# Kernel tuning notes

Measured on AMD Instinct MI355X. Metric: run time of the kernel, lower is better.

The kernel has to match this reference:

```python
import jax, jax.numpy as jnp
import numpy as np

N_AGENTS = 8
OBS = 64          # num_inputs // n_agents
HIDDEN = 128
NUM_OUT = 16
BATCH = 16384     # per-agent batch -> rows = BATCH * N_AGENTS = 131072


def setup_inputs() -> dict:
    key = jax.random.key(0)
    ks = jax.random.split(key, 9)
    s = lambda fan_in: 1.0 / np.sqrt(fan_in)
    inputs = jax.random.normal(ks[0], (BATCH * N_AGENTS, OBS), dtype=jnp.float32)
    w1  = jax.random.uniform(ks[1], (HIDDEN, OBS), jnp.float32, -s(OBS), s(OBS))
    b1  = jax.random.uniform(ks[2], (HIDDEN,), jnp.float32, -s(OBS), s(OBS))
    w1o = jax.random.uniform(ks[3], (HIDDEN, OBS), jnp.float32, -s(OBS), s(OBS))
    b1o = jax.random.uniform(ks[4], (HIDDEN,), jnp.float32, -s(OBS), s(OBS))
    w2  = jax.random.uniform(ks[5], (HIDDEN, 2 * HIDDEN), jnp.float32, -s(2 * HIDDEN), s(2 * HIDDEN))
    b2  = jax.random.uniform(ks[6], (HIDDEN,), jnp.float32, -s(2 * HIDDEN), s(2 * HIDDEN))
    wv  = jax.random.uniform(ks[7], (NUM_OUT, HIDDEN), jnp.float32, -s(HIDDEN), s(HIDDEN)) * 0.1
    bv  = jax.random.uniform(ks[8], (NUM_OUT,), jnp.float32, -s(HIDDEN), s(HIDDEN)) * 0.1
    return {"inputs": inputs, "w1": w1, "b1": b1, "w1o": w1o, "b1o": b1o,
            "w2": w2, "b2": b2, "wv": wv, "bv": bv}


def reference(inputs, w1, b1, w1o, b1o, w2, b2, wv, bv):
    n = N_AGENTS
    B = inputs.shape[0] // n
    obs = inputs.shape[1]
    # state_other: roll features by -1, then for each of n iterations take
    # [B, n, obs][:, 1:] and roll again (faithful to torch.roll/cat loop).
    rolled = jnp.roll(inputs, -1, axis=1)
    parts = []
    for _ in range(n):  # fixed small structural loop
        parts.append(rolled.reshape(B, n, obs)[:, 1:])
        rolled = jnp.roll(rolled, -1, axis=1)
    state_other = jnp.concatenate(parts, axis=1).reshape(B * n, n - 1, obs)

    h1 = jax.nn.relu(inputs @ w1.T + b1)                                   # [B*n, H]
    h1_other = jax.nn.relu(jnp.einsum('bno,ho->bnh', state_other, w1o) + b1o)  # [B*n, n-1, H]
    h1_summed = jnp.sum(h1_other, axis=1) / n                              # [B*n, H]
    h = jnp.concatenate([h1, h1_summed], axis=1)                           # [B*n, 2H]
    h2 = jax.nn.relu(h @ w2.T + b2)                                        # [B*n, H]
    return h2 @ wv.T + bv                                                  # [B*n, num_out]
```

## Files before the change

### kernel.cpp

```cpp
#include <hip/hip_runtime.h>
#include <stdint.h>
#include <stddef.h>


typedef __attribute__((ext_vector_type(8))) short short8;
typedef __attribute__((ext_vector_type(4))) float floatx4;
typedef __attribute__((ext_vector_type(4))) unsigned int uintx4;
typedef __attribute__((ext_vector_type(4))) float float4v;

static __device__ __forceinline__ unsigned int cvtpk(float lo, float hi) {
    unsigned int r;
    asm("v_cvt_pk_bf16_f32 %0, %1, %2" : "=v"(r) : "v"(lo), "v"(hi));
    return r;
}
static __device__ __forceinline__ unsigned short f2bf(float f) {
    return (unsigned short)cvtpk(f, f);
}

static __device__ __forceinline__ floatx4 mfma16(short8 a, short8 b, floatx4 c) {
    return __builtin_amdgcn_mfma_f32_16x16x32_bf16(a, b, c, 0, 0, 0);
}

__global__ void cvt_weights(const float* __restrict__ w1, const float* __restrict__ w1o,
                            const float* __restrict__ w2, const float* __restrict__ wv,
                            unsigned short* __restrict__ ws) {
    int i = blockIdx.x * 256 + threadIdx.x;
    float v;
    if (i < 8192)       v = w1[i];
    else if (i < 16384) v = w1o[i - 8192];
    else if (i < 49152) v = w2[i - 16384];
    else                v = wv[i - 49152];
    ws[i] = f2bf(v);
}

__launch_bounds__(256, 3)
__global__ void actor_fused(const float* __restrict__ X,
                            const unsigned short* __restrict__ ws,
                            const float* __restrict__ b1p,
                            const float* __restrict__ b1op,
                            const float* __restrict__ b2p,
                            const float* __restrict__ bvp,
                            float* __restrict__ out) {
    __shared__ __align__(16) unsigned char smem[51200];
    unsigned short (*Hc)[264] = (unsigned short (*)[264])(smem);
    unsigned short (*Xs)[72]  = (unsigned short (*)[72]) (smem + 33792);
    unsigned short (*H2)[136] = (unsigned short (*)[136])(smem + 33792);

    const int tid  = threadIdx.x;
    const int wid  = tid >> 6;
    const int lane = tid & 63;
    const int l15  = lane & 15;
    const int l16  = lane >> 4;
    const long R0  = (long)blockIdx.x * 64;

    const unsigned short* w1b  = ws;
    const unsigned short* w1ob = ws + 8192;
    const unsigned short* w2b  = ws + 16384;
    const unsigned short* wvb  = ws + 49152;

    short8 bo[8][2];
    float b1o_r[8];
    #pragma unroll
    for (int n = 0; n < 8; ++n) {
        const int h = n * 16 + l15;
        bo[n][0] = *(const short8*)(w1ob + h * 64 + l16 * 8);
        bo[n][1] = *(const short8*)(w1ob + h * 64 + 32 + l16 * 8);
        b1o_r[n] = b1op[h];
    }

    {
        const int r = tid >> 2, q = tid & 3;
        const float4v* src = (const float4v*)(X + (R0 + r) * 64 + q * 16);
        const float4v f0 = src[0], f1 = src[1], f2 = src[2], f3 = src[3];
        uintx4 lo, hi;
        lo.x = cvtpk(f0.x, f0.y); lo.y = cvtpk(f0.z, f0.w);
        lo.z = cvtpk(f1.x, f1.y); lo.w = cvtpk(f1.z, f1.w);
        hi.x = cvtpk(f2.x, f2.y); hi.y = cvtpk(f2.z, f2.w);
        hi.z = cvtpk(f3.x, f3.y); hi.w = cvtpk(f3.z, f3.w);
        *(uintx4*)(&Xs[r][q * 16])     = lo;
        *(uintx4*)(&Xs[r][q * 16 + 8]) = hi;
        if (q == 0) *(uintx4*)(&Xs[r][64]) = lo;
    }
    __syncthreads();

    const int xrow = 16 * wid + l15;
    uintx4 v0lo = *(const uintx4*)(&Xs[xrow][l16 * 8]);
    uintx4 v0hi = *(const uintx4*)(&Xs[xrow][l16 * 8 + 8]);
    uintx4 v1lo = *(const uintx4*)(&Xs[xrow][32 + l16 * 8]);
    uintx4 v1hi = *(const uintx4*)(&Xs[xrow][40 + l16 * 8]);
    unsigned int u0[8] = {v0lo.x, v0lo.y, v0lo.z, v0lo.w, v0hi.x, v0hi.y, v0hi.z, v0hi.w};
    unsigned int u1[8] = {v1lo.x, v1lo.y, v1lo.z, v1lo.w, v1hi.x, v1hi.y, v1hi.z, v1hi.w};

    const floatx4 zf = {0.f, 0.f, 0.f, 0.f};

    #pragma unroll
    for (int kx = 0; kx < 8; ++kx) {
        const int kk = kx + 1;
        const int c  = kk >> 1;
        union { unsigned int u[4]; short8 v; } A0, A1;
        #pragma unroll
        for (int d = 0; d < 4; ++d) {
            if (kk & 1) {
                A0.u[d] = (u0[d + c] >> 16) | (u0[d + c + 1] << 16);
                A1.u[d] = (u1[d + c] >> 16) | (u1[d + c + 1] << 16);
            } else {
                A0.u[d] = u0[d + c];
                A1.u[d] = u1[d + c];
            }
        }
        floatx4 acc[8];
        #pragma unroll
        for (int n = 0; n < 8; ++n) acc[n] = zf;
        #pragma unroll
        for (int n = 0; n < 8; ++n) {
            acc[n] = mfma16(A0.v, bo[n][0], acc[n]);
            acc[n] = mfma16(A1.v, bo[n][1], acc[n]);
        }
        #pragma unroll
        for (int n = 0; n < 8; ++n) {
            float r0 = fmaxf(acc[n].x + b1o_r[n], 0.f);
            float r1 = fmaxf(acc[n].y + b1o_r[n], 0.f);
            float r2 = fmaxf(acc[n].z + b1o_r[n], 0.f);
            float r3 = fmaxf(acc[n].w + b1o_r[n], 0.f);
            float t = r1 + r2 + r3 + (((l16 & 1) != 0) ? r0 : 0.f);
            float s = t + __shfl_xor(t, 16, 64);
            if ((lane & 16) == 0) {
                int row = 16 * wid + ((lane >> 5) << 3) + kx;
                Hc[row][128 + n * 16 + l15] = f2bf(s * 0.125f);
            }
        }
    }

    {
        short8 b1fr[8][2];
        float b1_r[8];
        #pragma unroll
        for (int n = 0; n < 8; ++n) {
            const int h = n * 16 + l15;
            b1fr[n][0] = *(const short8*)(w1b + h * 64 + l16 * 8);
            b1fr[n][1] = *(const short8*)(w1b + h * 64 + 32 + l16 * 8);
            b1_r[n]    = b1p[h];
        }
        union { unsigned int u[4]; short8 v; } A0, A1;
        #pragma unroll
        for (int d = 0; d < 4; ++d) { A0.u[d] = u0[d]; A1.u[d] = u1[d]; }
        floatx4 acc[8];
        #pragma unroll
        for (int n = 0; n < 8; ++n) acc[n] = zf;
        #pragma unroll
        for (int n = 0; n < 8; ++n) {
            acc[n] = mfma16(A0.v, b1fr[n][0], acc[n]);
            acc[n] = mfma16(A1.v, b1fr[n][1], acc[n]);
        }
        #pragma unroll
        for (int n = 0; n < 8; ++n) {
            #pragma unroll
            for (int r = 0; r < 4; ++r) {
                int row = 16 * wid + l16 * 4 + r;
                Hc[row][n * 16 + l15] = f2bf(fmaxf(acc[n][r] + b1_r[n], 0.f));
            }
        }
    }

    short8 w2f[2][8];
    float b2_r[2];
    #pragma unroll
    for (int n = 0; n < 2; ++n) {
        const int h = wid * 32 + n * 16 + l15;
        b2_r[n] = b2p[h];
        #pragma unroll
        for (int s = 0; s < 8; ++s)
            w2f[n][s] = *(const short8*)(w2b + (size_t)h * 256 + s * 32 + l16 * 8);
    }
    __syncthreads();

    #pragma unroll
    for (int mt = 0; mt < 4; ++mt) {
        floatx4 acc2[2] = {zf, zf};
        #pragma unroll
        for (int s = 0; s < 8; ++s) {
            short8 a = *(const short8*)(&Hc[mt * 16 + l15][s * 32 + l16 * 8]);
            acc2[0] = mfma16(a, w2f[0][s], acc2[0]);
            acc2[1] = mfma16(a, w2f[1][s], acc2[1]);
        }
        #pragma unroll
        for (int n = 0; n < 2; ++n) {
            #pragma unroll
            for (int r = 0; r < 4; ++r) {
                int row = mt * 16 + l16 * 4 + r;
                H2[row][wid * 32 + n * 16 + l15] = f2bf(fmaxf(acc2[n][r] + b2_r[n], 0.f));
            }
        }
    }

    short8 wvf[4];
    #pragma unroll
    for (int s = 0; s < 4; ++s)
        wvf[s] = *(const short8*)(wvb + l15 * 128 + s * 32 + l16 * 8);
    const float bv_r = bvp[l15];
    __syncthreads();

    {
        floatx4 acc4 = zf;
        #pragma unroll
        for (int s = 0; s < 4; ++s) {
            short8 a = *(const short8*)(&H2[wid * 16 + l15][s * 32 + l16 * 8]);
            acc4 = mfma16(a, wvf[s], acc4);
        }
        #pragma unroll
        for (int r = 0; r < 4; ++r) {
            long row = R0 + 16 * wid + l16 * 4 + r;
            out[row * 16 + l15] = acc4[r] + bv_r;
        }
    }
}

extern "C" void kernel_launch(void* const* d_in, const int* in_sizes, int n_in,
                              void* d_out, int out_size, void* d_ws, size_t ws_size,
                              hipStream_t stream) {
    (void)n_in; (void)out_size; (void)ws_size;
    const float* X   = (const float*)d_in[0];
    const float* w1  = (const float*)d_in[1];
    const float* b1  = (const float*)d_in[2];
    const float* w1o = (const float*)d_in[3];
    const float* b1o = (const float*)d_in[4];
    const float* w2  = (const float*)d_in[5];
    const float* b2  = (const float*)d_in[6];
    const float* wv  = (const float*)d_in[7];
    const float* bv  = (const float*)d_in[8];
    float* out = (float*)d_out;
    unsigned short* ws = (unsigned short*)d_ws;

    cvt_weights<<<200, 256, 0, stream>>>(w1, w1o, w2, wv, ws);

    const int rows   = in_sizes[0] / 64;
    const int blocks = rows / 64;
    actor_fused<<<blocks, 256, 0, stream>>>(X, ws, b1, b1o, b2, bv, out);
}
```

Measured before the change: 68.69 us.

## Load X directly into MFMA registers, fold biases and 1/n scale, shrink LDS

Each lane now reads its input rows from global memory straight into registers and converts them to bf16 there, dropping the X staging buffer in LDS and one barrier. The 1/n scale is folded into the converted w1o weights and b1o, and every bias is used as the initial MFMA accumulator instead of being added afterwards. LDS use falls from about 51 KB to about 33 KB and launch bounds move to 4 blocks per CU to raise occupancy. Because H2 now shares LDS with Hc, the layer-2 results are held in registers until an extra barrier, which raises register pressure and may cause spills at the tighter bound.

```diff
diff --git a/kernel.cpp b/kernel.cpp
--- a/kernel.cpp
+++ b/kernel.cpp
@@ -5,7 +5,6 @@
 
 typedef __attribute__((ext_vector_type(8))) short short8;
 typedef __attribute__((ext_vector_type(4))) float floatx4;
-typedef __attribute__((ext_vector_type(4))) unsigned int uintx4;
 typedef __attribute__((ext_vector_type(4))) float float4v;
 
 static __device__ __forceinline__ unsigned int cvtpk(float lo, float hi) {
@@ -27,13 +26,13 @@
     int i = blockIdx.x * 256 + threadIdx.x;
     float v;
     if (i < 8192)       v = w1[i];
-    else if (i < 16384) v = w1o[i - 8192];
+    else if (i < 16384) v = w1o[i - 8192] * 0.125f;
     else if (i < 49152) v = w2[i - 16384];
     else                v = wv[i - 49152];
     ws[i] = f2bf(v);
 }
 
-__launch_bounds__(256, 3)
+__launch_bounds__(256, 4)
 __global__ void actor_fused(const float* __restrict__ X,
                             const unsigned short* __restrict__ ws,
                             const float* __restrict__ b1p,
@@ -41,10 +40,9 @@
                             const float* __restrict__ b2p,
                             const float* __restrict__ bvp,
                             float* __restrict__ out) {
-    __shared__ __align__(16) unsigned char smem[51200];
-    unsigned short (*Hc)[264] = (unsigned short (*)[264])(smem);
-    unsigned short (*Xs)[72]  = (unsigned short (*)[72]) (smem + 33792);
-    unsigned short (*H2)[136] = (unsigned short (*)[136])(smem + 33792);
+    __shared__ __align__(16) unsigned char smem[33792];
+    unsigned short (*Hc)[264] = (unsigned short (*)[264])smem;
+    unsigned short (*H2)[136] = (unsigned short (*)[136])smem;
 
     const int tid  = threadIdx.x;
     const int wid  = tid >> 6;
@@ -58,6 +56,16 @@
     const unsigned short* w2b  = ws + 16384;
     const unsigned short* wvb  = ws + 49152;
 
+    const float* xp = X + (R0 + 16 * wid + l15) * 64;
+    float4v a0 = *(const float4v*)(xp + l16 * 8);
+    float4v a1 = *(const float4v*)(xp + l16 * 8 + 4);
+    float4v a2 = *(const float4v*)(xp + l16 * 8 + 8);
+    float4v a3 = *(const float4v*)(xp + l16 * 8 + 12);
+    float4v c0 = *(const float4v*)(xp + ((32 + l16 * 8) & 63));
+    float4v c1 = *(const float4v*)(xp + ((36 + l16 * 8) & 63));
+    float4v c2 = *(const float4v*)(xp + ((40 + l16 * 8) & 63));
+    float4v c3 = *(const float4v*)(xp + ((44 + l16 * 8) & 63));
+
     short8 bo[8][2];
     float b1o_r[8];
     #pragma unroll
@@ -65,33 +73,18 @@
         const int h = n * 16 + l15;
         bo[n][0] = *(const short8*)(w1ob + h * 64 + l16 * 8);
         bo[n][1] = *(const short8*)(w1ob + h * 64 + 32 + l16 * 8);
-        b1o_r[n] = b1op[h];
-    }
-
-    {
-        const int r = tid >> 2, q = tid & 3;
-        const float4v* src = (const float4v*)(X + (R0 + r) * 64 + q * 16);
-        const float4v f0 = src[0], f1 = src[1], f2 = src[2], f3 = src[3];
-        uintx4 lo, hi;
-        lo.x = cvtpk(f0.x, f0.y); lo.y = cvtpk(f0.z, f0.w);
-        lo.z = cvtpk(f1.x, f1.y); lo.w = cvtpk(f1.z, f1.w);
-        hi.x = cvtpk(f2.x, f2.y); hi.y = cvtpk(f2.z, f2.w);
-        hi.z = cvtpk(f3.x, f3.y); hi.w = cvtpk(f3.z, f3.w);
-        *(uintx4*)(&Xs[r][q * 16])     = lo;
-        *(uintx4*)(&Xs[r][q * 16 + 8]) = hi;
-        if (q == 0) *(uintx4*)(&Xs[r][64]) = lo;
-    }
-    __syncthreads();
-
-    const int xrow = 16 * wid + l15;
-    uintx4 v0lo = *(const uintx4*)(&Xs[xrow][l16 * 8]);
-    uintx4 v0hi = *(const uintx4*)(&Xs[xrow][l16 * 8 + 8]);
-    uintx4 v1lo = *(const uintx4*)(&Xs[xrow][32 + l16 * 8]);
-    uintx4 v1hi = *(const uintx4*)(&Xs[xrow][40 + l16 * 8]);
-    unsigned int u0[8] = {v0lo.x, v0lo.y, v0lo.z, v0lo.w, v0hi.x, v0hi.y, v0hi.z, v0hi.w};
-    unsigned int u1[8] = {v1lo.x, v1lo.y, v1lo.z, v1lo.w, v1hi.x, v1hi.y, v1hi.z, v1hi.w};
-
-    const floatx4 zf = {0.f, 0.f, 0.f, 0.f};
+        b1o_r[n] = 0.125f * b1op[h];
+    }
+
+    unsigned int u0[8], u1[8];
+    u0[0] = cvtpk(a0.x, a0.y); u0[1] = cvtpk(a0.z, a0.w);
+    u0[2] = cvtpk(a1.x, a1.y); u0[3] = cvtpk(a1.z, a1.w);
+    u0[4] = cvtpk(a2.x, a2.y); u0[5] = cvtpk(a2.z, a2.w);
+    u0[6] = cvtpk(a3.x, a3.y); u0[7] = cvtpk(a3.z, a3.w);
+    u1[0] = cvtpk(c0.x, c0.y); u1[1] = cvtpk(c0.z, c0.w);
+    u1[2] = cvtpk(c1.x, c1.y); u1[3] = cvtpk(c1.z, c1.w);
+    u1[4] = cvtpk(c2.x, c2.y); u1[5] = cvtpk(c2.z, c2.w);
+    u1[6] = cvtpk(c3.x, c3.y); u1[7] = cvtpk(c3.z, c3.w);
 
     #pragma unroll
     for (int kx = 0; kx < 8; ++kx) {
@@ -110,7 +103,10 @@
         }
         floatx4 acc[8];
         #pragma unroll
-        for (int n = 0; n < 8; ++n) acc[n] = zf;
+        for (int n = 0; n < 8; ++n) {
+            const float b = b1o_r[n];
+            acc[n] = (floatx4){b, b, b, b};
+        }
         #pragma unroll
         for (int n = 0; n < 8; ++n) {
             acc[n] = mfma16(A0.v, bo[n][0], acc[n]);
@@ -118,15 +114,15 @@
         }
         #pragma unroll
         for (int n = 0; n < 8; ++n) {
-            float r0 = fmaxf(acc[n].x + b1o_r[n], 0.f);
-            float r1 = fmaxf(acc[n].y + b1o_r[n], 0.f);
-            float r2 = fmaxf(acc[n].z + b1o_r[n], 0.f);
-            float r3 = fmaxf(acc[n].w + b1o_r[n], 0.f);
+            float r0 = fmaxf(acc[n].x, 0.f);
+            float r1 = fmaxf(acc[n].y, 0.f);
+            float r2 = fmaxf(acc[n].z, 0.f);
+            float r3 = fmaxf(acc[n].w, 0.f);
             float t = r1 + r2 + r3 + (((l16 & 1) != 0) ? r0 : 0.f);
             float s = t + __shfl_xor(t, 16, 64);
             if ((lane & 16) == 0) {
                 int row = 16 * wid + ((lane >> 5) << 3) + kx;
-                Hc[row][128 + n * 16 + l15] = f2bf(s * 0.125f);
+                Hc[row][128 + n * 16 + l15] = f2bf(s);
             }
         }
     }
@@ -146,7 +142,10 @@
         for (int d = 0; d < 4; ++d) { A0.u[d] = u0[d]; A1.u[d] = u1[d]; }
         floatx4 acc[8];
         #pragma unroll
-        for (int n = 0; n < 8; ++n) acc[n] = zf;
+        for (int n = 0; n < 8; ++n) {
+            const float b = b1_r[n];
+            acc[n] = (floatx4){b, b, b, b};
+        }
         #pragma unroll
         for (int n = 0; n < 8; ++n) {
             acc[n] = mfma16(A0.v, b1fr[n][0], acc[n]);
@@ -157,17 +156,19 @@
             #pragma unroll
             for (int r = 0; r < 4; ++r) {
                 int row = 16 * wid + l16 * 4 + r;
-                Hc[row][n * 16 + l15] = f2bf(fmaxf(acc[n][r] + b1_r[n], 0.f));
+                Hc[row][n * 16 + l15] = f2bf(fmaxf(acc[n][r], 0.f));
             }
         }
     }
 
     short8 w2f[2][8];
-    float b2_r[2];
+    floatx4 acc2[4][2];
     #pragma unroll
     for (int n = 0; n < 2; ++n) {
         const int h = wid * 32 + n * 16 + l15;
-        b2_r[n] = b2p[h];
+        const float b = b2p[h];
+        #pragma unroll
+        for (int mt = 0; mt < 4; ++mt) acc2[mt][n] = (floatx4){b, b, b, b};
         #pragma unroll
         for (int s = 0; s < 8; ++s)
             w2f[n][s] = *(const short8*)(w2b + (size_t)h * 256 + s * 32 + l16 * 8);
@@ -176,32 +177,37 @@
 
     #pragma unroll
     for (int mt = 0; mt < 4; ++mt) {
-        floatx4 acc2[2] = {zf, zf};
         #pragma unroll
         for (int s = 0; s < 8; ++s) {
             short8 a = *(const short8*)(&Hc[mt * 16 + l15][s * 32 + l16 * 8]);
-            acc2[0] = mfma16(a, w2f[0][s], acc2[0]);
-            acc2[1] = mfma16(a, w2f[1][s], acc2[1]);
-        }
+            acc2[mt][0] = mfma16(a, w2f[0][s], acc2[mt][0]);
+            acc2[mt][1] = mfma16(a, w2f[1][s], acc2[mt][1]);
+        }
+    }
+
+    short8 wvf[4];
+    #pragma unroll
+    for (int s = 0; s < 4; ++s)
+        wvf[s] = *(const short8*)(wvb + l15 * 128 + s * 32 + l16 * 8);
+    const float bv_r = bvp[l15];
+
+    __syncthreads();
+
+    #pragma unroll
+    for (int mt = 0; mt < 4; ++mt) {
         #pragma unroll
         for (int n = 0; n < 2; ++n) {
             #pragma unroll
             for (int r = 0; r < 4; ++r) {
                 int row = mt * 16 + l16 * 4 + r;
-                H2[row][wid * 32 + n * 16 + l15] = f2bf(fmaxf(acc2[n][r] + b2_r[n], 0.f));
-            }
-        }
-    }
-
-    short8 wvf[4];
-    #pragma unroll
-    for (int s = 0; s < 4; ++s)
-        wvf[s] = *(const short8*)(wvb + l15 * 128 + s * 32 + l16 * 8);
-    const float bv_r = bvp[l15];
+                H2[row][wid * 32 + n * 16 + l15] = f2bf(fmaxf(acc2[mt][n][r], 0.f));
+            }
+        }
+    }
     __syncthreads();
 
     {
-        floatx4 acc4 = zf;
+        floatx4 acc4 = (floatx4){bv_r, bv_r, bv_r, bv_r};
         #pragma unroll
         for (int s = 0; s < 4; ++s) {
             short8 a = *(const short8*)(&H2[wid * 16 + l15][s * 32 + l16 * 8]);
@@ -210,7 +216,7 @@
         #pragma unroll
         for (int r = 0; r < 4; ++r) {
             long row = R0 + 16 * wid + l16 * 4 + r;
-            out[row * 16 + l15] = acc4[r] + bv_r;
+            out[row * 16 + l15] = acc4[r];
         }
     }
 }
```

New measurement: 171.2 us. 2.49x slower.

## Restructure fused actor kernel into single-wave blocks of 16 rows without barriers

Applied to the files above, without the earlier changes.

Each block is now one 64-lane wavefront handling 16 rows, so all __syncthreads are removed and shared memory shrinks to 8 KB with XOR-swizzled layouts for the hidden buffers. Weights for the first layers load in two phases to reduce register pressure. Layer 2 streams W2 fragments from global/L2 per block instead of keeping them in registers. The 1/8 mean scale is folded into w1o and biases are used as accumulator initial values. In exchange, blocks are four times as many and weight reads per row rise, since each wave re-reads all of W2 for only 16 rows.

```diff
diff --git a/kernel.cpp b/kernel.cpp
--- a/kernel.cpp
+++ b/kernel.cpp
@@ -16,10 +16,13 @@
 static __device__ __forceinline__ unsigned short f2bf(float f) {
     return (unsigned short)cvtpk(f, f);
 }
-
 static __device__ __forceinline__ floatx4 mfma16(short8 a, short8 b, floatx4 c) {
     return __builtin_amdgcn_mfma_f32_16x16x32_bf16(a, b, c, 0, 0, 0);
 }
+
+#define XSI(r, c) ((r) * 72 + (c))
+#define HCI(r, c) (((((r) << 5) | ((c) >> 3)) ^ ((r) & 7)) * 8 + ((c) & 7))
+#define H2I(r, c) (((((r) << 4) | ((c) >> 3)) ^ ((r) & 7)) * 8 + ((c) & 7))
 
 __global__ void cvt_weights(const float* __restrict__ w1, const float* __restrict__ w1o,
                             const float* __restrict__ w2, const float* __restrict__ wv,
@@ -27,13 +30,13 @@
     int i = blockIdx.x * 256 + threadIdx.x;
     float v;
     if (i < 8192)       v = w1[i];
-    else if (i < 16384) v = w1o[i - 8192];
+    else if (i < 16384) v = w1o[i - 8192] * 0.125f;
     else if (i < 49152) v = w2[i - 16384];
     else                v = wv[i - 49152];
     ws[i] = f2bf(v);
 }
 
-__launch_bounds__(256, 3)
+__launch_bounds__(64, 4)
 __global__ void actor_fused(const float* __restrict__ X,
                             const unsigned short* __restrict__ ws,
                             const float* __restrict__ b1p,
@@ -41,35 +44,20 @@
                             const float* __restrict__ b2p,
                             const float* __restrict__ bvp,
                             float* __restrict__ out) {
-    __shared__ __align__(16) unsigned char smem[51200];
-    unsigned short (*Hc)[264] = (unsigned short (*)[264])(smem);
-    unsigned short (*Xs)[72]  = (unsigned short (*)[72]) (smem + 33792);
-    unsigned short (*H2)[136] = (unsigned short (*)[136])(smem + 33792);
-
-    const int tid  = threadIdx.x;
-    const int wid  = tid >> 6;
-    const int lane = tid & 63;
+    __shared__ __align__(16) unsigned short P[4096];
+
+    const int lane = threadIdx.x;
     const int l15  = lane & 15;
     const int l16  = lane >> 4;
-    const long R0  = (long)blockIdx.x * 64;
+    const long R0  = (long)blockIdx.x * 16;
 
     const unsigned short* w1b  = ws;
     const unsigned short* w1ob = ws + 8192;
     const unsigned short* w2b  = ws + 16384;
     const unsigned short* wvb  = ws + 49152;
 
-    short8 bo[8][2];
-    float b1o_r[8];
-    #pragma unroll
-    for (int n = 0; n < 8; ++n) {
-        const int h = n * 16 + l15;
-        bo[n][0] = *(const short8*)(w1ob + h * 64 + l16 * 8);
-        bo[n][1] = *(const short8*)(w1ob + h * 64 + 32 + l16 * 8);
-        b1o_r[n] = b1op[h];
-    }
-
     {
-        const int r = tid >> 2, q = tid & 3;
+        const int r = lane >> 2, q = lane & 3;
         const float4v* src = (const float4v*)(X + (R0 + r) * 64 + q * 16);
         const float4v f0 = src[0], f1 = src[1], f2 = src[2], f3 = src[3];
         uintx4 lo, hi;
@@ -77,119 +65,128 @@
         lo.z = cvtpk(f1.x, f1.y); lo.w = cvtpk(f1.z, f1.w);
         hi.x = cvtpk(f2.x, f2.y); hi.y = cvtpk(f2.z, f2.w);
         hi.z = cvtpk(f3.x, f3.y); hi.w = cvtpk(f3.z, f3.w);
-        *(uintx4*)(&Xs[r][q * 16])     = lo;
-        *(uintx4*)(&Xs[r][q * 16 + 8]) = hi;
-        if (q == 0) *(uintx4*)(&Xs[r][64]) = lo;
-    }
-    __syncthreads();
-
-    const int xrow = 16 * wid + l15;
-    uintx4 v0lo = *(const uintx4*)(&Xs[xrow][l16 * 8]);
-    uintx4 v0hi = *(const uintx4*)(&Xs[xrow][l16 * 8 + 8]);
-    uintx4 v1lo = *(const uintx4*)(&Xs[xrow][32 + l16 * 8]);
-    uintx4 v1hi = *(const uintx4*)(&Xs[xrow][40 + l16 * 8]);
+        *(uintx4*)(&P[XSI(r, q * 16)])     = lo;
+        *(uintx4*)(&P[XSI(r, q * 16 + 8)]) = hi;
+        if (q == 0) *(uintx4*)(&P[XSI(r, 64)]) = lo;
+    }
+
+    uintx4 v0lo = *(const uintx4*)(&P[XSI(l15, l16 * 8)]);
+    uintx4 v0hi = *(const uintx4*)(&P[XSI(l15, l16 * 8 + 8)]);
+    uintx4 v1lo = *(const uintx4*)(&P[XSI(l15, 32 + l16 * 8)]);
+    uintx4 v1hi = *(const uintx4*)(&P[XSI(l15, 40 + l16 * 8)]);
     unsigned int u0[8] = {v0lo.x, v0lo.y, v0lo.z, v0lo.w, v0hi.x, v0hi.y, v0hi.z, v0hi.w};
     unsigned int u1[8] = {v1lo.x, v1lo.y, v1lo.z, v1lo.w, v1hi.x, v1hi.y, v1hi.z, v1hi.w};
 
-    const floatx4 zf = {0.f, 0.f, 0.f, 0.f};
-
+    #pragma unroll 1
+    for (int ph = 0; ph < 2; ++ph) {
+        short8 bw[4][2];
+        float  bia[4];
+        #pragma unroll
+        for (int i = 0; i < 4; ++i) {
+            const int h = (ph * 4 + i) * 16 + l15;
+            bw[i][0] = *(const short8*)(w1ob + h * 64 + l16 * 8);
+            bw[i][1] = *(const short8*)(w1ob + h * 64 + 32 + l16 * 8);
+            bia[i]   = 0.125f * b1op[h];
+        }
+        #pragma unroll
+        for (int kx = 0; kx < 8; ++kx) {
+            const int kk = kx + 1;
+            const int c  = kk >> 1;
+            union { unsigned int u[4]; short8 v; } A0, A1;
+            #pragma unroll
+            for (int d = 0; d < 4; ++d) {
+                if (kk & 1) {
+                    A0.u[d] = (u0[d + c] >> 16) | (u0[d + c + 1] << 16);
+                    A1.u[d] = (u1[d + c] >> 16) | (u1[d + c + 1] << 16);
+                } else {
+                    A0.u[d] = u0[d + c];
+                    A1.u[d] = u1[d + c];
+                }
+            }
+            floatx4 acc[4];
+            #pragma unroll
+            for (int i = 0; i < 4; ++i) {
+                const float b = bia[i];
+                acc[i] = (floatx4){b, b, b, b};
+            }
+            #pragma unroll
+            for (int i = 0; i < 4; ++i) {
+                acc[i] = mfma16(A0.v, bw[i][0], acc[i]);
+                acc[i] = mfma16(A1.v, bw[i][1], acc[i]);
+            }
+            #pragma unroll
+            for (int i = 0; i < 4; ++i) {
+                float r0 = fmaxf(acc[i].x, 0.f);
+                float r1 = fmaxf(acc[i].y, 0.f);
+                float r2 = fmaxf(acc[i].z, 0.f);
+                float r3 = fmaxf(acc[i].w, 0.f);
+                float t = r1 + r2 + r3 + (((l16 & 1) != 0) ? r0 : 0.f);
+                float s = t + __shfl_xor(t, 16, 64);
+                if ((lane & 16) == 0) {
+                    int row = ((lane >> 5) << 3) + kx;
+                    P[HCI(row, 128 + (ph * 4 + i) * 16 + l15)] = f2bf(s);
+                }
+            }
+        }
+    }
+
+    #pragma unroll 1
+    for (int ph = 0; ph < 2; ++ph) {
+        short8 bw[4][2];
+        float  bia[4];
+        #pragma unroll
+        for (int i = 0; i < 4; ++i) {
+            const int h = (ph * 4 + i) * 16 + l15;
+            bw[i][0] = *(const short8*)(w1b + h * 64 + l16 * 8);
+            bw[i][1] = *(const short8*)(w1b + h * 64 + 32 + l16 * 8);
+            bia[i]   = b1p[h];
+        }
+        union { unsigned int u[4]; short8 v; } A0, A1;
+        #pragma unroll
+        for (int d = 0; d < 4; ++d) { A0.u[d] = u0[d]; A1.u[d] = u1[d]; }
+        floatx4 acc[4];
+        #pragma unroll
+        for (int i = 0; i < 4; ++i) {
+            const float b = bia[i];
+            acc[i] = (floatx4){b, b, b, b};
+        }
+        #pragma unroll
+        for (int i = 0; i < 4; ++i) {
+            acc[i] = mfma16(A0.v, bw[i][0], acc[i]);
+            acc[i] = mfma16(A1.v, bw[i][1], acc[i]);
+        }
+        #pragma unroll
+        for (int i = 0; i < 4; ++i) {
+            #pragma unroll
+            for (int r = 0; r < 4; ++r) {
+                P[HCI(l16 * 4 + r, (ph * 4 + i) * 16 + l15)] = f2bf(fmaxf(acc[i][r], 0.f));
+            }
+        }
+    }
+
+    short8 af[8];
     #pragma unroll
-    for (int kx = 0; kx < 8; ++kx) {
-        const int kk = kx + 1;
-        const int c  = kk >> 1;
-        union { unsigned int u[4]; short8 v; } A0, A1;
-        #pragma unroll
-        for (int d = 0; d < 4; ++d) {
-            if (kk & 1) {
-                A0.u[d] = (u0[d + c] >> 16) | (u0[d + c + 1] << 16);
-                A1.u[d] = (u1[d + c] >> 16) | (u1[d + c + 1] << 16);
-            } else {
-                A0.u[d] = u0[d + c];
-                A1.u[d] = u1[d + c];
-            }
-        }
-        floatx4 acc[8];
-        #pragma unroll
-        for (int n = 0; n < 8; ++n) acc[n] = zf;
-        #pragma unroll
-        for (int n = 0; n < 8; ++n) {
-            acc[n] = mfma16(A0.v, bo[n][0], acc[n]);
-            acc[n] = mfma16(A1.v, bo[n][1], acc[n]);
-        }
-        #pragma unroll
-        for (int n = 0; n < 8; ++n) {
-            float r0 = fmaxf(acc[n].x + b1o_r[n], 0.f);
-            float r1 = fmaxf(acc[n].y + b1o_r[n], 0.f);
-            float r2 = fmaxf(acc[n].z + b1o_r[n], 0.f);
-            float r3 = fmaxf(acc[n].w + b1o_r[n], 0.f);
-            float t = r1 + r2 + r3 + (((l16 & 1) != 0) ? r0 : 0.f);
-            float s = t + __shfl_xor(t, 16, 64);
-            if ((lane & 16) == 0) {
-                int row = 16 * wid + ((lane >> 5) << 3) + kx;
-                Hc[row][128 + n * 16 + l15] = f2bf(s * 0.125f);
-            }
-        }
-    }
-
-    {
-        short8 b1fr[8][2];
-        float b1_r[8];
-        #pragma unroll
-        for (int n = 0; n < 8; ++n) {
-            const int h = n * 16 + l15;
-            b1fr[n][0] = *(const short8*)(w1b + h * 64 + l16 * 8);
-            b1fr[n][1] = *(const short8*)(w1b + h * 64 + 32 + l16 * 8);
-            b1_r[n]    = b1p[h];
-        }
-        union { unsigned int u[4]; short8 v; } A0, A1;
-        #pragma unroll
-        for (int d = 0; d < 4; ++d) { A0.u[d] = u0[d]; A1.u[d] = u1[d]; }
-        floatx4 acc[8];
-        #pragma unroll
-        for (int n = 0; n < 8; ++n) acc[n] = zf;
-        #pragma unroll
-        for (int n = 0; n < 8; ++n) {
-            acc[n] = mfma16(A0.v, b1fr[n][0], acc[n]);
-            acc[n] = mfma16(A1.v, b1fr[n][1], acc[n]);
-        }
-        #pragma unroll
-        for (int n = 0; n < 8; ++n) {
-            #pragma unroll
-            for (int r = 0; r < 4; ++r) {
-                int row = 16 * wid + l16 * 4 + r;
-                Hc[row][n * 16 + l15] = f2bf(fmaxf(acc[n][r] + b1_r[n], 0.f));
-            }
-        }
-    }
-
-    short8 w2f[2][8];
-    float b2_r[2];
-    #pragma unroll
-    for (int n = 0; n < 2; ++n) {
-        const int h = wid * 32 + n * 16 + l15;
-        b2_r[n] = b2p[h];
-        #pragma unroll
-        for (int s = 0; s < 8; ++s)
-            w2f[n][s] = *(const short8*)(w2b + (size_t)h * 256 + s * 32 + l16 * 8);
-    }
-    __syncthreads();
-
-    #pragma unroll
-    for (int mt = 0; mt < 4; ++mt) {
-        floatx4 acc2[2] = {zf, zf};
+    for (int s = 0; s < 8; ++s)
+        af[s] = *(const short8*)(&P[HCI(l15, s * 32 + l16 * 8)]);
+
+    #pragma unroll 1
+    for (int ng = 0; ng < 4; ++ng) {
+        const int n0 = 2 * ng, n1 = 2 * ng + 1;
+        const float bb0 = b2p[n0 * 16 + l15];
+        const float bb1 = b2p[n1 * 16 + l15];
+        floatx4 a0 = (floatx4){bb0, bb0, bb0, bb0};
+        floatx4 a1 = (floatx4){bb1, bb1, bb1, bb1};
         #pragma unroll
         for (int s = 0; s < 8; ++s) {
-            short8 a = *(const short8*)(&Hc[mt * 16 + l15][s * 32 + l16 * 8]);
-            acc2[0] = mfma16(a, w2f[0][s], acc2[0]);
-            acc2[1] = mfma16(a, w2f[1][s], acc2[1]);
-        }
-        #pragma unroll
-        for (int n = 0; n < 2; ++n) {
-            #pragma unroll
-            for (int r = 0; r < 4; ++r) {
-                int row = mt * 16 + l16 * 4 + r;
-                H2[row][wid * 32 + n * 16 + l15] = f2bf(fmaxf(acc2[n][r] + b2_r[n], 0.f));
-            }
+            short8 w0 = *(const short8*)(w2b + (size_t)(n0 * 16 + l15) * 256 + s * 32 + l16 * 8);
+            short8 w1f = *(const short8*)(w2b + (size_t)(n1 * 16 + l15) * 256 + s * 32 + l16 * 8);
+            a0 = mfma16(af[s], w0, a0);
+            a1 = mfma16(af[s], w1f, a1);
+        }
+        #pragma unroll
+        for (int r = 0; r < 4; ++r) {
+            P[H2I(l16 * 4 + r, n0 * 16 + l15)] = f2bf(fmaxf(a0[r], 0.f));
+            P[H2I(l16 * 4 + r, n1 * 16 + l15)] = f2bf(fmaxf(a1[r], 0.f));
         }
     }
 
@@ -198,19 +195,18 @@
     for (int s = 0; s < 4; ++s)
         wvf[s] = *(const short8*)(wvb + l15 * 128 + s * 32 + l16 * 8);
     const float bv_r = bvp[l15];
-    __syncthreads();
 
     {
-        floatx4 acc4 = zf;
+        floatx4 acc4 = (floatx4){bv_r, bv_r, bv_r, bv_r};
         #pragma unroll
         for (int s = 0; s < 4; ++s) {
-            short8 a = *(const short8*)(&H2[wid * 16 + l15][s * 32 + l16 * 8]);
+            short8 a = *(const short8*)(&P[H2I(l15, s * 32 + l16 * 8)]);
             acc4 = mfma16(a, wvf[s], acc4);
         }
         #pragma unroll
         for (int r = 0; r < 4; ++r) {
-            long row = R0 + 16 * wid + l16 * 4 + r;
-            out[row * 16 + l15] = acc4[r] + bv_r;
+            long row = R0 + l16 * 4 + r;
+            out[row * 16 + l15] = acc4[r];
         }
     }
 }
@@ -234,6 +230,6 @@
     cvt_weights<<<200, 256, 0, stream>>>(w1, w1o, w2, wv, ws);
 
     const int rows   = in_sizes[0] / 64;
-    const int blocks = rows / 64;
-    actor_fused<<<blocks, 256, 0, stream>>>(X, ws, b1, b1o, b2, bv, out);
-}
+    const int blocks = rows / 16;
+    actor_fused<<<blocks, 64, 0, stream>>>(X, ws, b1, b1o, b2, bv, out);
+}
```

Result: slower. 128.7 us (+87.3%).
